# Performance work log

Measured on AMD Instinct MI355X. Metric: run time of the kernel, lower is better.

## Reference

```python
import jax, jax.numpy as jnp
import numpy as np

ENC_H = 512      # encoder_hidden_dim -> encoder_out feature = 2*ENC_H
DEC_H = 512      # decoder_hidden_dim
B, S = 32, 2048  # batch, max_seq_len


def setup_inputs() -> dict:
    key = jax.random.key(0)
    k1, k2, k3, k4, k5, k6, k7 = jax.random.split(key, 7)
    encoder_out = jax.random.normal(k1, (B, S, 2 * ENC_H), dtype=jnp.float32)
    hidden = jax.random.normal(k2, (B, DEC_H), dtype=jnp.float32)
    lengths = jax.random.randint(k3, (B,), 1, S + 1, dtype=jnp.int64)
    in_dim = 2 * ENC_H + DEC_H
    # torch nn.Linear default init scale
    attn_w = jax.random.uniform(k4, (DEC_H, in_dim), jnp.float32, -1.0, 1.0) / np.sqrt(in_dim)
    attn_b = jax.random.uniform(k5, (DEC_H,), jnp.float32, -1.0, 1.0) / np.sqrt(in_dim)
    v_w = jax.random.uniform(k6, (1, DEC_H), jnp.float32, -1.0, 1.0) / np.sqrt(DEC_H)
    v_b = jax.random.uniform(k7, (1,), jnp.float32, -1.0, 1.0) / np.sqrt(DEC_H)
    return {"encoder_out": encoder_out, "hidden": hidden, "lengths": lengths,
            "attn_w": attn_w, "attn_b": attn_b, "v_w": v_w, "v_b": v_b}


def reference(encoder_out, hidden, lengths, attn_w, attn_b, v_w, v_b):
    # encoder_out: [B,S,2E], hidden: [B,D], lengths: [B]
    Bc, Sc, _ = encoder_out.shape
    h = jnp.broadcast_to(hidden[:, None, :], (Bc, Sc, hidden.shape[-1]))
    temp = jnp.concatenate([h, encoder_out], axis=2)           # [B,S,D+2E]
    e = jnp.tanh(jnp.einsum('bsf,df->bsd', temp, attn_w) + attn_b)  # [B,S,D]
    scores = jnp.einsum('bsd,d->bs', e, v_w[0]) + v_b[0]       # [B,S]
    mask = jnp.arange(Sc)[None, :] < lengths[:, None]          # [B,S]
    scores = jnp.where(mask, scores, -jnp.inf)
    energy = jax.nn.softmax(scores, axis=1)                    # softmax over valid positions
    energy = jnp.where(mask, energy, 0.0)                      # padded positions stay exactly 0
    context = jnp.einsum('bs,bse->be', energy, encoder_out)    # [B,2E]
    return context
```

## Files before the change

kernel.cpp:

```cpp
#include <hip/hip_runtime.h>
#include <hip/hip_bf16.h>
#include <math.h>

typedef __attribute__((ext_vector_type(8))) short short8;
typedef __attribute__((ext_vector_type(16))) float f32x16;

static constexpr int B  = 32;
static constexpr int S  = 2048;
static constexpr int D  = 512;
static constexpr int KE = 1024;
static constexpr int IN = 1536;

__device__ __forceinline__ unsigned pk2(float lo, float hi) {
    __hip_bfloat162 t = __float22bfloat162_rn(make_float2(lo, hi));
    unsigned u;
    __builtin_memcpy(&u, &t, 4);
    return u;
}

__device__ __forceinline__ short8 pack8(float4 f0, float4 f1) {
    unsigned u[4] = { pk2(f0.x, f0.y), pk2(f0.z, f0.w), pk2(f1.x, f1.y), pk2(f1.z, f1.w) };
    short8 r;
    __builtin_memcpy(&r, u, 16);
    return r;
}

__device__ __forceinline__ float tanh_fast(float x) {
    float e = __expf(2.0f * x);
    return (e - 1.0f) * __builtin_amdgcn_rcpf(e + 1.0f);
}

typedef const __attribute__((address_space(1))) unsigned int guint;
typedef __attribute__((address_space(3))) unsigned int luint;
__device__ __forceinline__ void gload_lds16(const void* g, void* l) {
    __builtin_amdgcn_global_load_lds((guint*)g, (luint*)l, 16, 0, 0);
}

__global__ void k_prep(const float* __restrict__ attn_w,
                       const float* __restrict__ hidden,
                       const float* __restrict__ attn_b,
                       unsigned short* __restrict__ Bf,
                       float* __restrict__ u) {
    if (blockIdx.x < 256) {
        int o = blockIdx.x * 256 + threadIdx.x;
        int l6  = o & 63;
        int grp = o >> 6;
        int d = (grp & 15) * 32 + (l6 & 31);
        int k = (grp >> 4) * 16 + (l6 >> 5) * 8;
        const float* src = attn_w + (size_t)d * IN + 512 + k;
        float4 f0 = *(const float4*)src;
        float4 f1 = *(const float4*)(src + 4);
        ((short8*)Bf)[o] = pack8(f0, f1);
    } else {
        int bx = blockIdx.x - 256;
        int b  = bx >> 1;
        int dh = bx & 1;
        int w  = threadIdx.x >> 6;
        int l  = threadIdx.x & 63;
        int j  = l & 15;
        int dsub = l >> 4;
        const float* h = hidden + b * D;
        float4 hv[8];
        #pragma unroll
        for (int i = 0; i < 8; i++) hv[i] = *(const float4*)(h + i * 64 + j * 4);
        #pragma unroll
        for (int p = 0; p < 16; p++) {
            int d = dh * 256 + p * 16 + w * 4 + dsub;
            const float* wr = attn_w + (size_t)d * IN + j * 4;
            float a = 0.f;
            #pragma unroll
            for (int i = 0; i < 8; i++) {
                float4 wv = *(const float4*)(wr + i * 64);
                a += hv[i].x * wv.x + hv[i].y * wv.y + hv[i].z * wv.z + hv[i].w * wv.w;
            }
            #pragma unroll
            for (int off = 8; off >= 1; off >>= 1) a += __shfl_xor(a, off);
            if (j == 0) u[b * D + d] = a + attn_b[d];
        }
    }
}

#define LOADB(K, DST) do {                                     \
    _Pragma("unroll")                                          \
    for (int _jt = 0; _jt < 4; _jt++)                          \
        DST[_jt] = bb[(size_t)(K) * 1024 + _jt * 64];          \
} while (0)

__global__ __launch_bounds__(256, 2) void k_fused(
    const float* __restrict__ enc, const unsigned short* __restrict__ Bfrag,
    const float* __restrict__ u, const float* __restrict__ v_w,
    const float* __restrict__ v_b, const int* __restrict__ lengths,
    float* __restrict__ num, float* __restrict__ den)
{
    __shared__ float4 ldsA[2][1024];
    __shared__ float sPart[4][64];
    __shared__ float sExp[64];

    const int b   = blockIdx.y;
    const int s0  = blockIdx.x * 64;
    const int len = lengths[b];
    if (s0 >= len) return;

    const int tid = threadIdx.x;
    const int w   = tid >> 6;
    const int l   = tid & 63;

    const float* encb = enc + ((size_t)b * S + s0) * KE;

    const int rsub = l >> 4;
    const int xorv = (l & 15) ^ (w * 4 + rsub);
    const float* aSrc = encb + (size_t)(w * 4 + rsub) * KE + 4 * xorv;

    const short8* bb = (const short8*)Bfrag + (w * 4) * 64 + l;

    f32x16 acc[2][4];
    #pragma unroll
    for (int mt = 0; mt < 2; mt++)
        #pragma unroll
        for (int jt = 0; jt < 4; jt++)
            #pragma unroll
            for (int e = 0; e < 16; e++) acc[mt][jt][e] = 0.f;

    short8 pb[2][4];
    LOADB(0, pb[0]);
    LOADB(1, pb[1]);

    const int m0  = l & 31;
    const int x15 = m0 & 15;
    const int hi2 = (l >> 5) * 2;

    #pragma unroll
    for (int i = 0; i < 4; i++)
        gload_lds16(aSrc + (size_t)i * 16 * KE, (void*)&ldsA[0][(i * 4 + w) * 64]);

    #pragma unroll 1
    for (int c = 0; c < 16; ++c) {
        __syncthreads();
        if (c < 15) {
            const float* src = aSrc + (c + 1) * 64;
            float4* bufn = ldsA[(c + 1) & 1];
            #pragma unroll
            for (int i = 0; i < 4; i++)
                gload_lds16(src + (size_t)i * 16 * KE, (void*)&bufn[(i * 4 + w) * 64]);
        }
        const float4* bf = (const float4*)ldsA[c & 1];
        #pragma unroll
        for (int t2 = 0; t2 < 4; ++t2) {
            const int sq = t2 * 4 + hi2;
            const int p0 = sq ^ x15;
            const int p1 = (sq + 1) ^ x15;
            float4 f00 = bf[m0 * 16 + p0];
            float4 f01 = bf[m0 * 16 + p1];
            float4 f10 = bf[(m0 + 32) * 16 + p0];
            float4 f11 = bf[(m0 + 32) * 16 + p1];
            short8 a0 = pack8(f00, f01);
            short8 a1 = pack8(f10, f11);
            const int bp = t2 & 1;
            #pragma unroll
            for (int jt = 0; jt < 4; jt++) {
                acc[0][jt] = __builtin_amdgcn_mfma_f32_32x32x16_bf16(a0, pb[bp][jt], acc[0][jt], 0, 0, 0);
                acc[1][jt] = __builtin_amdgcn_mfma_f32_32x32x16_bf16(a1, pb[bp][jt], acc[1][jt], 0, 0, 0);
            }
            LOADB((c * 4 + t2 + 2) & 63, pb[bp]);
        }
    }

    float vv[4], uu[4];
    const float* ub = u + b * D;
    #pragma unroll
    for (int jt = 0; jt < 4; jt++) {
        int d = w * 128 + jt * 32 + (l & 31);
        vv[jt] = v_w[d];
        uu[jt] = ub[d];
    }
    float red[2][16];
    #pragma unroll
    for (int mt = 0; mt < 2; mt++)
        #pragma unroll
        for (int r = 0; r < 16; r++) {
            float s = 0.f;
            #pragma unroll
            for (int jt = 0; jt < 4; jt++)
                s += vv[jt] * tanh_fast(acc[mt][jt][r] + uu[jt]);
            red[mt][r] = s;
        }
    #pragma unroll
    for (int off = 16; off >= 1; off >>= 1)
        #pragma unroll
        for (int mt = 0; mt < 2; mt++)
            #pragma unroll
            for (int r = 0; r < 16; r++)
                red[mt][r] += __shfl_xor(red[mt][r], off);
    if ((l & 31) == 0) {
        int hb = (l >> 5) * 4;
        #pragma unroll
        for (int mt = 0; mt < 2; mt++)
            #pragma unroll
            for (int r = 0; r < 16; r++)
                sPart[w][mt * 32 + (r & 3) + 8 * (r >> 2) + hb] = red[mt][r];
    }
    __syncthreads();

    if (tid < 64) {
        float sc = sPart[0][tid] + sPart[1][tid] + sPart[2][tid] + sPart[3][tid] + v_b[0];
        float wexp = (s0 + tid < len) ? __expf(sc) : 0.f;
        sExp[tid] = wexp;
        #pragma unroll
        for (int off = 32; off >= 1; off >>= 1) wexp += __shfl_xor(wexp, off);
        if (tid == 0) atomicAdd(den + b, wexp);
    }
    __syncthreads();

    const float4* e4 = (const float4*)encb;
    float4 cacc[4];
    #pragma unroll
    for (int j = 0; j < 4; j++) cacc[j] = make_float4(0.f, 0.f, 0.f, 0.f);
    #pragma unroll
    for (int i = 0; i < 16; i++) {
        #pragma unroll
        for (int j = 0; j < 4; j++) {
            float wgt = sExp[i * 4 + j];
            float4 v = e4[(size_t)(i * 4 + j) * 256 + tid];
            cacc[j].x += wgt * v.x; cacc[j].y += wgt * v.y;
            cacc[j].z += wgt * v.z; cacc[j].w += wgt * v.w;
        }
    }
    #pragma unroll
    for (int j = 1; j < 4; j++) {
        cacc[0].x += cacc[j].x; cacc[0].y += cacc[j].y;
        cacc[0].z += cacc[j].z; cacc[0].w += cacc[j].w;
    }
    float* o = num + b * KE + tid * 4;
    atomicAdd(o + 0, cacc[0].x);
    atomicAdd(o + 1, cacc[0].y);
    atomicAdd(o + 2, cacc[0].z);
    atomicAdd(o + 3, cacc[0].w);
}

__global__ void k_norm(const float* __restrict__ num, const float* __restrict__ den,
                       float* __restrict__ out) {
    int b = blockIdx.x;
    int t = threadIdx.x;
    float inv = 1.f / den[b];
    float4 v = ((const float4*)(num + b * KE))[t];
    v.x *= inv; v.y *= inv; v.z *= inv; v.w *= inv;
    ((float4*)(out + b * KE))[t] = v;
}

extern "C" void kernel_launch(void* const* d_in, const int* in_sizes, int n_in,
                              void* d_out, int out_size, void* d_ws, size_t ws_size,
                              hipStream_t stream) {
    const float* enc    = (const float*)d_in[0];
    const float* hidden = (const float*)d_in[1];
    const int*   lengths= (const int*)d_in[2];
    const float* attn_w = (const float*)d_in[3];
    const float* attn_b = (const float*)d_in[4];
    const float* v_w    = (const float*)d_in[5];
    const float* v_b    = (const float*)d_in[6];
    float* out = (float*)d_out;

    float* ws  = (float*)d_ws;
    float* u   = ws;
    float* num = u + B * D;
    float* den = num + B * KE;
    unsigned short* Bf = (unsigned short*)(den + 32);

    (void)hipMemsetAsync(num, 0, (size_t)(B * KE + B) * sizeof(float), stream);
    k_prep <<<dim3(320), 256, 0, stream>>>(attn_w, hidden, attn_b, Bf, u);
    k_fused<<<dim3(S / 64, B), 256, 0, stream>>>(enc, Bf, u, v_w, v_b, lengths, num, den);
    k_norm <<<dim3(B), 256, 0, stream>>>(num, den, out);
}
```

Baseline: 444.9 us.

## Double K-chunk size in fused attention GEMM and fold memset into prep kernel

The K-loop of the fused kernel now stages 128-column chunks of encoder_out per LDS buffer instead of 64, halving the iteration count and barrier count. The swizzle and load addressing are adjusted to the wider rows, and sPart/sExp now alias the LDS A buffer. Zeroing of the num/den accumulators moves from a separate hipMemsetAsync into the k_prep kernel, removing one launch. LDS use doubles to 64KB per block, which may limit co-residency to fewer blocks per CU than the launch bounds request.

```diff
diff --git a/kernel.cpp b/kernel.cpp
--- a/kernel.cpp
+++ b/kernel.cpp
@@ -40,7 +40,9 @@
                        const float* __restrict__ hidden,
                        const float* __restrict__ attn_b,
                        unsigned short* __restrict__ Bf,
-                       float* __restrict__ u) {
+                       float* __restrict__ u,
+                       float* __restrict__ num,
+                       float* __restrict__ den) {
     if (blockIdx.x < 256) {
         int o = blockIdx.x * 256 + threadIdx.x;
         int l6  = o & 63;
@@ -53,6 +55,11 @@
         ((short8*)Bf)[o] = pack8(f0, f1);
     } else {
         int bx = blockIdx.x - 256;
+        {
+            int gid = bx * 256 + threadIdx.x;
+            ((float2*)num)[gid] = make_float2(0.f, 0.f);
+            if (bx == 0 && threadIdx.x < 32) den[threadIdx.x] = 0.f;
+        }
         int b  = bx >> 1;
         int dh = bx & 1;
         int w  = threadIdx.x >> 6;
@@ -92,9 +99,9 @@
     const float* __restrict__ v_b, const int* __restrict__ lengths,
     float* __restrict__ num, float* __restrict__ den)
 {
-    __shared__ float4 ldsA[2][1024];
-    __shared__ float sPart[4][64];
-    __shared__ float sExp[64];
+    __shared__ float4 ldsA[2][2048];
+    float* sPart = (float*)&ldsA[0][0];
+    float* sExp  = sPart + 256;
 
     const int b   = blockIdx.y;
     const int s0  = blockIdx.x * 64;
@@ -107,9 +114,9 @@
 
     const float* encb = enc + ((size_t)b * S + s0) * KE;
 
-    const int rsub = l >> 4;
-    const int xorv = (l & 15) ^ (w * 4 + rsub);
-    const float* aSrc = encb + (size_t)(w * 4 + rsub) * KE + 4 * xorv;
+    const int rlo  = l >> 5;
+    const int xv   = (l & 31) ^ (2 * w + rlo);
+    const float* aSrc = encb + (size_t)(2 * w + rlo) * KE + 4 * xv;
 
     const short8* bb = (const short8*)Bfrag + (w * 4) * 64 + l;
 
@@ -126,42 +133,42 @@
     LOADB(1, pb[1]);
 
     const int m0  = l & 31;
-    const int x15 = m0 & 15;
+    const int xr  = m0 & 7;
     const int hi2 = (l >> 5) * 2;
 
     #pragma unroll
-    for (int i = 0; i < 4; i++)
-        gload_lds16(aSrc + (size_t)i * 16 * KE, (void*)&ldsA[0][(i * 4 + w) * 64]);
+    for (int i = 0; i < 8; i++)
+        gload_lds16(aSrc + (size_t)i * 8 * KE, (void*)&ldsA[0][(i * 4 + w) * 64]);
 
     #pragma unroll 1
-    for (int c = 0; c < 16; ++c) {
+    for (int c = 0; c < 8; ++c) {
         __syncthreads();
-        if (c < 15) {
-            const float* src = aSrc + (c + 1) * 64;
+        if (c < 7) {
+            const float* src = aSrc + (c + 1) * 128;
             float4* bufn = ldsA[(c + 1) & 1];
             #pragma unroll
-            for (int i = 0; i < 4; i++)
-                gload_lds16(src + (size_t)i * 16 * KE, (void*)&bufn[(i * 4 + w) * 64]);
-        }
-        const float4* bf = (const float4*)ldsA[c & 1];
-        #pragma unroll
-        for (int t2 = 0; t2 < 4; ++t2) {
-            const int sq = t2 * 4 + hi2;
-            const int p0 = sq ^ x15;
-            const int p1 = (sq + 1) ^ x15;
-            float4 f00 = bf[m0 * 16 + p0];
-            float4 f01 = bf[m0 * 16 + p1];
-            float4 f10 = bf[(m0 + 32) * 16 + p0];
-            float4 f11 = bf[(m0 + 32) * 16 + p1];
+            for (int i = 0; i < 8; i++)
+                gload_lds16(src + (size_t)i * 8 * KE, (void*)&bufn[(i * 4 + w) * 64]);
+        }
+        const float4* bf = &ldsA[c & 1][0];
+        #pragma unroll
+        for (int t = 0; t < 8; ++t) {
+            const int s0l = t * 4 + hi2;
+            const int p0  = s0l ^ xr;
+            const int p1  = (s0l + 1) ^ xr;
+            float4 f00 = bf[m0 * 32 + p0];
+            float4 f01 = bf[m0 * 32 + p1];
+            float4 f10 = bf[(m0 + 32) * 32 + p0];
+            float4 f11 = bf[(m0 + 32) * 32 + p1];
             short8 a0 = pack8(f00, f01);
             short8 a1 = pack8(f10, f11);
-            const int bp = t2 & 1;
+            const int bp = t & 1;
             #pragma unroll
             for (int jt = 0; jt < 4; jt++) {
                 acc[0][jt] = __builtin_amdgcn_mfma_f32_32x32x16_bf16(a0, pb[bp][jt], acc[0][jt], 0, 0, 0);
                 acc[1][jt] = __builtin_amdgcn_mfma_f32_32x32x16_bf16(a1, pb[bp][jt], acc[1][jt], 0, 0, 0);
             }
-            LOADB((c * 4 + t2 + 2) & 63, pb[bp]);
+            LOADB((c * 8 + t + 2) & 63, pb[bp]);
         }
     }
 
@@ -197,12 +204,12 @@
         for (int mt = 0; mt < 2; mt++)
             #pragma unroll
             for (int r = 0; r < 16; r++)
-                sPart[w][mt * 32 + (r & 3) + 8 * (r >> 2) + hb] = red[mt][r];
+                sPart[w * 64 + mt * 32 + (r & 3) + 8 * (r >> 2) + hb] = red[mt][r];
     }
     __syncthreads();
 
     if (tid < 64) {
-        float sc = sPart[0][tid] + sPart[1][tid] + sPart[2][tid] + sPart[3][tid] + v_b[0];
+        float sc = sPart[tid] + sPart[64 + tid] + sPart[128 + tid] + sPart[192 + tid] + v_b[0];
         float wexp = (s0 + tid < len) ? __expf(sc) : 0.f;
         sExp[tid] = wexp;
         #pragma unroll
@@ -265,8 +272,7 @@
     float* den = num + B * KE;
     unsigned short* Bf = (unsigned short*)(den + 32);
 
-    (void)hipMemsetAsync(num, 0, (size_t)(B * KE + B) * sizeof(float), stream);
-    k_prep <<<dim3(320), 256, 0, stream>>>(attn_w, hidden, attn_b, Bf, u);
+    k_prep <<<dim3(320), 256, 0, stream>>>(attn_w, hidden, attn_b, Bf, u, num, den);
     k_fused<<<dim3(S / 64, B), 256, 0, stream>>>(enc, Bf, u, v_w, v_b, lengths, num, den);
     k_norm <<<dim3(B), 256, 0, stream>>>(num, den, out);
 }
```

Measured after the change: 439.0 us. About the same (-1.3%).
